# Performance work log

Hardware: AMD Instinct MI355X
Metric: run time of the kernel (lower is better)

The kernel has to match this reference:

```python
import jax, jax.numpy as jnp
import numpy as np

NUM_LAYERS = 6
D = 16           # physical_dim == bond_dim (required for multi-layer consistency)
B, S, FIN = 128, 2048, 128


def setup_inputs() -> dict:
    key = jax.random.key(0)
    k0, k1, k2, k3 = jax.random.split(key, 4)
    return {
        "sequence": jax.random.normal(k0, (B, S, FIN), jnp.float32),
        "W_emb": jax.random.normal(k1, (FIN, D), jnp.float32) * 0.05,
        "b_emb": jnp.zeros((D,), jnp.float32),
        "u": jax.random.normal(k2, (NUM_LAYERS, D, D, D, D), jnp.float32) * 0.1,
        "w": jax.random.normal(k3, (NUM_LAYERS, D, D, D), jnp.float32) * 0.1,
    }


def _ent_entropy(sA, sB):
    # sA: (B, pA, d), sB: (B, pB, d)
    corr = jnp.einsum('bik,bjk->bij', sA, sB)          # (B, pA, pB)
    s = jnp.linalg.svd(corr, compute_uv=False)          # (B, min(pA,pB))
    sn = s / (jnp.sum(s, axis=1, keepdims=True) + 1e-8)
    return -jnp.sum(sn * jnp.log(sn + 1e-8), axis=1)    # (B,)


def _phi_q(sites):
    # sites: (B, n, d), n >= 4 and even
    n = sites.shape[1]
    mid = n // 2
    S_int = _ent_entropy(sites[:, :mid], sites[:, mid:])
    A, Bp = sites[:, :mid], sites[:, mid:]
    S1 = _ent_entropy(A[:, :mid // 2], A[:, mid // 2:])
    S2 = _ent_entropy(Bp[:, :(n - mid) // 2], Bp[:, (n - mid) // 2:])
    return jnp.maximum(S_int - (S1 + S2), 0.0)


def _apply_layer(sites, u_l, w_l):
    # sites: (B, n, d) with n even. Disentangle adjacent pairs, then coarse-grain.
    b, n, d = sites.shape
    s = sites.reshape(b, n // 2, 2, d)
    # disentangler: einsum('ijkl,bi,bj->bkl') batched over pairs p
    comb = jnp.einsum('ijkl,bpi,bpj->bpkl', u_l, s[:, :, 0], s[:, :, 1])
    o1 = comb.mean(axis=3)   # mean over l -> (b, p, k)
    o2 = comb.mean(axis=2)   # mean over k -> (b, p, l)
    # isometry acts on consecutive disentangled pairs (o1_i, o2_i)
    return jnp.einsum('aij,bpi,bpj->bpa', w_l, o1, o2)  # (b, n//2, bond)


def reference(sequence, W_emb, b_emb, u, w):
    emb = sequence @ W_emb + b_emb                       # (B, S, D)
    norm = jnp.linalg.norm(emb, axis=-1, keepdims=True)
    sites = emb / jnp.maximum(norm, 1e-12)               # F.normalize(dim=-1)
    for l in range(NUM_LAYERS):
        sites = _apply_layer(sites, u[l], w[l])
    phi_q = _phi_q(sites)
    return sites, phi_q
```

## Files before the change

### kernel.cpp

```cpp
#include <hip/hip_runtime.h>
#include <hip/hip_bf16.h>
#include <math.h>

#define BATCH 128
#define SEQ   2048
#define FIN   128
#define DD    16
#define NLAYERS 6
#define SST   20
#define SWEEPS 8

#define BUFA_F  (BATCH*SEQ*DD)
#define BUFB_F  (BATCH*(SEQ/2)*DD)
#define COEF_OFF (BUFA_F + BUFB_F)
#define ENT_OFF  (COEF_OFF + NLAYERS*12288)

__global__ __launch_bounds__(256) void k_front(const float* __restrict__ seq,
                                               const float* __restrict__ W,
                                               const float* __restrict__ bias,
                                               const float* __restrict__ u,
                                               const float* __restrict__ w,
                                               float* __restrict__ coef,
                                               float* __restrict__ out) {
    __shared__ float sW[2048];
    __shared__ float sR[64*132];
    int t = threadIdx.x;
    if (blockIdx.x < 6) {
        int l  = blockIdx.x;
        int ij = t;
        const float* ub = u + (size_t)l*65536 + (size_t)ij*256;
        float a1[16], a2[16];
#pragma unroll
        for (int k = 0; k < 16; ++k) { a1[k] = 0.0f; a2[k] = 0.0f; }
#pragma unroll
        for (int k = 0; k < 16; ++k) {
#pragma unroll
            for (int z = 0; z < 16; ++z) {
                float v = ub[k*16 + z];
                a1[k] += v;
                a2[z] += v;
            }
        }
        float* ucb = coef + (size_t)l*12288 + ij*32;
#pragma unroll
        for (int k = 0; k < 16; ++k) {
            ucb[k]      = a1[k]*(1.0f/16.0f);
            ucb[16 + k] = a2[k]*(1.0f/16.0f);
        }
        const float* wb = w + (size_t)l*4096;
        float* wtb = coef + (size_t)l*12288 + 8192 + ij*16;
#pragma unroll
        for (int a = 0; a < 16; ++a) wtb[a] = wb[a*256 + ij];
        return;
    }
    size_t rowbase = (size_t)(blockIdx.x - 6) * 64;
    for (int x = t; x < 2048; x += 256) sW[x] = W[x];
    {
        const float4* seq4 = (const float4*)seq + rowbase*32;
#pragma unroll
        for (int it = 0; it < 8; ++it) {
            int idx = t + it*256;
            int r = idx >> 5, kk = idx & 31;
            *(float4*)&sR[r*132 + kk*4] = seq4[idx];
        }
    }
    int q = t & 3, lr = t >> 2;
    float acc[4];
    {
        float4 bv = *(const float4*)(bias + q*4);
        acc[0] = bv.x; acc[1] = bv.y; acc[2] = bv.z; acc[3] = bv.w;
    }
    __syncthreads();

#pragma unroll 8
    for (int kk = 0; kk < 32; ++kk) {
        float4 rv = *(const float4*)&sR[lr*132 + kk*4];
        float rc[4] = { rv.x, rv.y, rv.z, rv.w };
#pragma unroll
        for (int c = 0; c < 4; ++c) {
            float4 wv = *(const float4*)&sW[(kk*4 + c)*16 + q*4];
            float s = rc[c];
            acc[0] = fmaf(s, wv.x, acc[0]);
            acc[1] = fmaf(s, wv.y, acc[1]);
            acc[2] = fmaf(s, wv.z, acc[2]);
            acc[3] = fmaf(s, wv.w, acc[3]);
        }
    }
    float p = 0.0f;
#pragma unroll
    for (int j = 0; j < 4; ++j) p = fmaf(acc[j], acc[j], p);
    p += __shfl_xor(p, 1);
    p += __shfl_xor(p, 2);
    float inv = 1.0f / fmaxf(sqrtf(p), 1e-12f);
    *(float4*)(out + (rowbase + lr)*16 + q*4) = make_float4(acc[0]*inv, acc[1]*inv,
                                                            acc[2]*inv, acc[3]*inv);
}

__global__ __launch_bounds__(256) void k_layer(const float* __restrict__ in,
                                               float* __restrict__ outp,
                                               const float* __restrict__ coefl) {
    __shared__ float cbuf[8192];
    __shared__ float spl[64*36];
    int t = threadIdx.x;
    int og = t & 7, pg = t >> 3;
    int lane = t & 63, base = lane & ~7;

    const float4* wtf = (const float4*)(coefl + 8192);
    float4 wr0 = wtf[0*256 + t];
    float4 wr1 = wtf[1*256 + t];
    float4 wr2 = wtf[2*256 + t];
    float4 wr3 = wtf[3*256 + t];

    {
        const float4* ucf = (const float4*)coefl;
        float4* c4 = (float4*)cbuf;
#pragma unroll
        for (int it = 0; it < 8; ++it) c4[it*256 + t] = ucf[it*256 + t];
    }
    {
        const float4* ing = (const float4*)in + (size_t)blockIdx.x*512;
        float4 v0 = ing[t];
        float4 v1 = ing[t + 256];
        *(float4*)&spl[(t >> 3)*36 + (t & 7)*4]        = v0;
        *(float4*)&spl[((t >> 3) + 32)*36 + (t & 7)*4] = v1;
    }
    __syncthreads();

    float s1v[2][16];
#pragma unroll
    for (int pp = 0; pp < 2; ++pp) {
        int p = pg + pp*32;
#pragma unroll
        for (int g = 0; g < 4; ++g) {
            float4 v = *(const float4*)&spl[p*36 + 16 + g*4];
            s1v[pp][g*4+0]=v.x; s1v[pp][g*4+1]=v.y; s1v[pp][g*4+2]=v.z; s1v[pp][g*4+3]=v.w;
        }
    }

    float accv[2][4];
    accv[0][0]=0.f; accv[0][1]=0.f; accv[0][2]=0.f; accv[0][3]=0.f;
    accv[1][0]=0.f; accv[1][1]=0.f; accv[1][2]=0.f; accv[1][3]=0.f;

    for (int i = 0; i < 16; ++i) {
        float s0a = spl[pg*36 + i];
        float s0b = spl[(pg + 32)*36 + i];
        const float4* uc = (const float4*)&cbuf[i*512] + og;
#pragma unroll
        for (int j = 0; j < 16; ++j) {
            float4 cv = uc[j*8];
            float pa = s0a * s1v[0][j];
            float pb = s0b * s1v[1][j];
            accv[0][0] = fmaf(pa, cv.x, accv[0][0]);
            accv[0][1] = fmaf(pa, cv.y, accv[0][1]);
            accv[0][2] = fmaf(pa, cv.z, accv[0][2]);
            accv[0][3] = fmaf(pa, cv.w, accv[0][3]);
            accv[1][0] = fmaf(pb, cv.x, accv[1][0]);
            accv[1][1] = fmaf(pb, cv.y, accv[1][1]);
            accv[1][2] = fmaf(pb, cv.z, accv[1][2]);
            accv[1][3] = fmaf(pb, cv.w, accv[1][3]);
        }
    }
    __syncthreads();
    {
        float4* c4 = (float4*)cbuf;
        c4[0*256 + t] = wr0;
        c4[1*256 + t] = wr1;
        c4[2*256 + t] = wr2;
        c4[3*256 + t] = wr3;
    }
    __syncthreads();

    float o2f[2][16];
#pragma unroll
    for (int j = 0; j < 16; ++j) {
        int src = base + 4 + (j >> 2);
        o2f[0][j] = __shfl(accv[0][j & 3], src, 64);
        o2f[1][j] = __shfl(accv[1][j & 3], src, 64);
    }

    float r0a = 0.f, r1a = 0.f, r0b = 0.f, r1b = 0.f;
    for (int grp = 0; grp < 4; ++grp) {
#pragma unroll
        for (int c = 0; c < 4; ++c) {
            float o1a = __shfl(accv[0][c], base + grp, 64);
            float o1b = __shfl(accv[1][c], base + grp, 64);
            const float2* wrow = (const float2*)&cbuf[(grp*4 + c)*256] + og;
#pragma unroll
            for (int j = 0; j < 16; ++j) {
                float2 wv = wrow[j*8];
                float qa = o1a * o2f[0][j];
                float qb = o1b * o2f[1][j];
                r0a = fmaf(qa, wv.x, r0a);
                r1a = fmaf(qa, wv.y, r1a);
                r0b = fmaf(qb, wv.x, r0b);
                r1b = fmaf(qb, wv.y, r1b);
            }
        }
    }

    size_t gp = (size_t)blockIdx.x*64;
    *(float2*)&outp[(gp + pg)*16 + og*2]      = make_float2(r0a, r1a);
    *(float2*)&outp[(gp + pg + 32)*16 + og*2] = make_float2(r0b, r1b);
}

template<int P, bool LAST>
__device__ __forceinline__ void layer_body(float* sL, const float* coef,
                                           float* outp, int npg, int t, int bid) {
    int og = t & 7, pg = t >> 3;
    int lane = t & 63, base = lane & ~7;
    bool act = pg < npg;

    float accv[P][4];
    float s1v[P][16];
#pragma unroll
    for (int pp = 0; pp < P; ++pp) { accv[pp][0]=0.f; accv[pp][1]=0.f; accv[pp][2]=0.f; accv[pp][3]=0.f; }

    if (act) {
#pragma unroll
        for (int pp = 0; pp < P; ++pp) {
            int r = 2*(pg + pp*32) + 1;
#pragma unroll
            for (int g = 0; g < 4; ++g) {
                float4 v = *(const float4*)&sL[r*SST + g*4];
                s1v[pp][g*4+0]=v.x; s1v[pp][g*4+1]=v.y; s1v[pp][g*4+2]=v.z; s1v[pp][g*4+3]=v.w;
            }
        }
        for (int i = 0; i < 16; ++i) {
            float s0[P];
#pragma unroll
            for (int pp = 0; pp < P; ++pp) s0[pp] = sL[(2*(pg + pp*32))*SST + i];
            const float4* uc = (const float4*)&coef[i*512] + og;
#pragma unroll
            for (int j = 0; j < 16; ++j) {
                float4 cv = uc[j*8];
#pragma unroll
                for (int pp = 0; pp < P; ++pp) {
                    float p = s0[pp] * s1v[pp][j];
                    accv[pp][0] = fmaf(p, cv.x, accv[pp][0]);
                    accv[pp][1] = fmaf(p, cv.y, accv[pp][1]);
                    accv[pp][2] = fmaf(p, cv.z, accv[pp][2]);
                    accv[pp][3] = fmaf(p, cv.w, accv[pp][3]);
                }
            }
        }
    }
    __syncthreads();

    if (act) {
        float o2f[P][16];
#pragma unroll
        for (int j = 0; j < 16; ++j) {
            int src = base + 4 + (j >> 2);
#pragma unroll
            for (int pp = 0; pp < P; ++pp)
                o2f[pp][j] = __shfl(accv[pp][j & 3], src, 64);
        }
        float r0[P], r1[P];
#pragma unroll
        for (int pp = 0; pp < P; ++pp) { r0[pp] = 0.f; r1[pp] = 0.f; }
        for (int grp = 0; grp < 4; ++grp) {
#pragma unroll
            for (int c = 0; c < 4; ++c) {
                float o1i[P];
#pragma unroll
                for (int pp = 0; pp < P; ++pp)
                    o1i[pp] = __shfl(accv[pp][c], base + grp, 64);
#pragma unroll
                for (int j = 0; j < 16; ++j) {
                    float2 wv = *(const float2*)&coef[8192 + ((grp*4+c)*16 + j)*16 + og*2];
#pragma unroll
                    for (int pp = 0; pp < P; ++pp) {
                        float q = o1i[pp] * o2f[pp][j];
                        r0[pp] = fmaf(q, wv.x, r0[pp]);
                        r1[pp] = fmaf(q, wv.y, r1[pp]);
                    }
                }
            }
        }
        if (LAST) {
#pragma unroll
            for (int pp = 0; pp < P; ++pp) {
                int p = pg + pp*32;
                *(float2*)&outp[((size_t)bid*32 + p)*16 + og*2] = make_float2(r0[pp], r1[pp]);
            }
        } else {
#pragma unroll
            for (int pp = 0; pp < P; ++pp) {
                int p = pg + pp*32;
                *(float2*)&sL[p*SST + og*2] = make_float2(r0[pp], r1[pp]);
            }
        }
    }
    __syncthreads();
}

__global__ __launch_bounds__(256) void k_tail(const float* __restrict__ in,
                                              const float* __restrict__ coefg,
                                              float* __restrict__ outp) {
    __shared__ float coef[12288];
    __shared__ float sL[256*SST];
    int t = threadIdx.x, bid = blockIdx.x;

    const float4* in4 = (const float4*)in + (size_t)bid*1024;
#pragma unroll
    for (int it = 0; it < 4; ++it) {
        int f = it*256 + t;
        *(float4*)&sL[(f >> 2)*SST + (f & 3)*4] = in4[f];
    }
#pragma unroll 1
    for (int l = 0; l < 3; ++l) {
        const float4* src = (const float4*)(coefg + (size_t)(3 + l)*12288);
        __syncthreads();
        for (int x = t; x < 3072; x += 256) ((float4*)coef)[x] = src[x];
        __syncthreads();
        switch (l) {
            case 0: layer_body<4,false>(sL, coef, outp, 32, t, bid); break;
            case 1: layer_body<2,false>(sL, coef, outp, 32, t, bid); break;
            case 2: layer_body<1,true >(sL, coef, outp, 32, t, bid); break;
        }
    }
}

__device__ __forceinline__ void rot_cs(float al, float be, float ga, float& c, float& s) {
    float ze = (be - al) / (2.0f * ga);
    float tt = copysignf(1.0f, ze) / (fabsf(ze) + sqrtf(1.0f + ze*ze));
    c = 1.0f / sqrtf(1.0f + tt*tt);
    s = c * tt;
}

__global__ __launch_bounds__(64) void k_phi(const float* __restrict__ sites,
                                            float* __restrict__ ent) {
    __shared__ float S[512];
    __shared__ float C[256];
    __shared__ float sv[16];
    int bid = blockIdx.x;
    int role = bid >> 7;
    int b = bid & 127;
    int t = threadIdx.x;
    const float* sp = sites + (size_t)b*512;

    if (role == 0) {
        for (int x = t; x < 512; x += 64) S[x] = sp[x];
        __syncthreads();
        for (int e = t; e < 256; e += 64) {
            int i = e & 15, j = e >> 4;
            float a = 0.0f;
            for (int k = 0; k < 16; ++k) a = fmaf(S[i*16+k], S[(16+j)*16+k], a);
            C[j*16 + i] = a;
        }
        __syncthreads();
        for (int sw = 0; sw < SWEEPS; ++sw) {
            for (int r = 0; r < 15; ++r) {
                int pr = t >> 3, sub = t & 7;
                int p, q;
                if (pr == 0) { p = 15; q = r; }
                else { p = (r + pr) % 15; q = (r + 15 - pr) % 15; }
                float u0 = C[p*16 + 2*sub],   u1v = C[p*16 + 2*sub + 1];
                float v0 = C[q*16 + 2*sub],   v1v = C[q*16 + 2*sub + 1];
                float al = u0*u0 + u1v*u1v;
                float be = v0*v0 + v1v*v1v;
                float ga = u0*v0 + u1v*v1v;
                al += __shfl_xor(al,1); al += __shfl_xor(al,2); al += __shfl_xor(al,4);
                be += __shfl_xor(be,1); be += __shfl_xor(be,2); be += __shfl_xor(be,4);
                ga += __shfl_xor(ga,1); ga += __shfl_xor(ga,2); ga += __shfl_xor(ga,4);
                if (ga != 0.0f) {
                    float c, s; rot_cs(al, be, ga, c, s);
                    C[p*16 + 2*sub]     = fmaf(c, u0, -s*v0);
                    C[p*16 + 2*sub + 1] = fmaf(c, u1v, -s*v1v);
                    C[q*16 + 2*sub]     = fmaf(s, u0,  c*v0);
                    C[q*16 + 2*sub + 1] = fmaf(s, u1v, c*v1v);
                }
                __syncthreads();
            }
        }
        if (t < 16) {
            float s2 = 0.0f;
            for (int rr = 0; rr < 16; ++rr) { float v = C[t*16+rr]; s2 = fmaf(v, v, s2); }
            sv[t] = sqrtf(s2);
        }
        __syncthreads();
        if (t == 0) {
            float sum = 0.0f;
            for (int i2 = 0; i2 < 16; ++i2) sum += sv[i2];
            float den = sum + 1e-8f;
            float e2 = 0.0f;
            for (int i2 = 0; i2 < 16; ++i2) {
                float sn = sv[i2] / den;
                e2 -= sn * logf(sn + 1e-8f);
            }
            ent[b] = e2;
        }
    } else {
        int ro = (role == 1) ? 0 : 256;
        for (int x = t; x < 256; x += 64) S[x] = sp[ro + x];
        __syncthreads();
        if (t < 64) {
            int i = t & 7, j = t >> 3;
            float a = 0.0f;
            for (int k = 0; k < 16; ++k) a = fmaf(S[i*16+k], S[(8+j)*16+k], a);
            C[j*8 + i] = a;
        }
        __syncthreads();
        for (int sw = 0; sw < SWEEPS; ++sw) {
            for (int r = 0; r < 7; ++r) {
                if (t < 32) {
                    int pr = t >> 3, sub = t & 7;
                    int p, q;
                    if (pr == 0) { p = 7; q = r; }
                    else { p = (r + pr) % 7; q = (r + 7 - pr) % 7; }
                    float uu = C[p*8 + sub], vv = C[q*8 + sub];
                    float al = uu*uu, be = vv*vv, ga = uu*vv;
                    al += __shfl_xor(al,1); al += __shfl_xor(al,2); al += __shfl_xor(al,4);
                    be += __shfl_xor(be,1); be += __shfl_xor(be,2); be += __shfl_xor(be,4);
                    ga += __shfl_xor(ga,1); ga += __shfl_xor(ga,2); ga += __shfl_xor(ga,4);
                    if (ga != 0.0f) {
                        float c, s; rot_cs(al, be, ga, c, s);
                        C[p*8 + sub] = fmaf(c, uu, -s*vv);
                        C[q*8 + sub] = fmaf(s, uu,  c*vv);
                    }
                }
                __syncthreads();
            }
        }
        if (t < 8) {
            float s2 = 0.0f;
            for (int rr = 0; rr < 8; ++rr) { float v = C[t*8+rr]; s2 = fmaf(v, v, s2); }
            sv[t] = sqrtf(s2);
        }
        __syncthreads();
        if (t == 0) {
            float sum = 0.0f;
            for (int i2 = 0; i2 < 8; ++i2) sum += sv[i2];
            float den = sum + 1e-8f;
            float e2 = 0.0f;
            for (int i2 = 0; i2 < 8; ++i2) {
                float sn = sv[i2] / den;
                e2 -= sn * logf(sn + 1e-8f);
            }
            ent[role*128 + b] = e2;
        }
    }
}

__global__ __launch_bounds__(128) void k_phi2(const float* __restrict__ ent,
                                              float* __restrict__ phi) {
    int b = threadIdx.x;
    phi[b] = fmaxf(ent[b] - (ent[128 + b] + ent[256 + b]), 0.0f);
}

extern "C" void kernel_launch(void* const* d_in, const int* in_sizes, int n_in,
                              void* d_out, int out_size, void* d_ws, size_t ws_size,
                              hipStream_t stream) {
    const float* seq  = (const float*)d_in[0];
    const float* W    = (const float*)d_in[1];
    const float* bias = (const float*)d_in[2];
    const float* u    = (const float*)d_in[3];
    const float* w    = (const float*)d_in[4];
    float* out = (float*)d_out;
    float* ws  = (float*)d_ws;

    float* bufA  = ws;
    float* bufB  = ws + BUFA_F;
    float* coefw = ws + COEF_OFF;
    float* entb  = ws + ENT_OFF;

    k_front<<<6 + (BATCH*SEQ)/64, 256, 0, stream>>>(seq, W, bias, u, w, coefw, bufA);

    k_layer<<<2048, 256, 0, stream>>>(bufA, bufB, coefw + 0*12288);
    k_layer<<<1024, 256, 0, stream>>>(bufB, bufA, coefw + 1*12288);
    k_layer<<< 512, 256, 0, stream>>>(bufA, bufB, coefw + 2*12288);
    k_tail <<< 128, 256, 0, stream>>>(bufB, coefw, out);

    k_phi <<<3*BATCH, 64, 0, stream>>>(out, entb);
    k_phi2<<<1, 128, 0, stream>>>(entb, out + BATCH*32*DD);
}
```

Baseline: 211.5 us.

## Read sequence rows directly from global memory in embedding kernel, two rows per thread

The embedding front kernel no longer stages 64 input rows in shared memory. Each thread now streams float4s of its rows straight from global memory and computes 4 output columns for two rows, so each block covers 128 rows. The row norm is reduced through a small shared buffer instead of shuffles. This removes the large shared-memory staging and its occupancy cost, but each lane now reads a separate 512-byte row stride, so global loads are poorly coalesced and four waves re-read the same rows.

```diff
diff --git a/kernel.cpp b/kernel.cpp
--- a/kernel.cpp
+++ b/kernel.cpp
@@ -23,7 +23,7 @@
                                                float* __restrict__ coef,
                                                float* __restrict__ out) {
     __shared__ float sW[2048];
-    __shared__ float sR[64*132];
+    __shared__ float psum[128*5 + 4];
     int t = threadIdx.x;
     if (blockIdx.x < 6) {
         int l  = blockIdx.x;
@@ -53,47 +53,52 @@
         for (int a = 0; a < 16; ++a) wtb[a] = wb[a*256 + ij];
         return;
     }
-    size_t rowbase = (size_t)(blockIdx.x - 6) * 64;
-    for (int x = t; x < 2048; x += 256) sW[x] = W[x];
-    {
-        const float4* seq4 = (const float4*)seq + rowbase*32;
-#pragma unroll
-        for (int it = 0; it < 8; ++it) {
-            int idx = t + it*256;
-            int r = idx >> 5, kk = idx & 31;
-            *(float4*)&sR[r*132 + kk*4] = seq4[idx];
-        }
-    }
-    int q = t & 3, lr = t >> 2;
-    float acc[4];
-    {
-        float4 bv = *(const float4*)(bias + q*4);
-        acc[0] = bv.x; acc[1] = bv.y; acc[2] = bv.z; acc[3] = bv.w;
-    }
-    __syncthreads();
-
+    int bid  = blockIdx.x - 6;
+    int lane = t & 63;
+    int q    = t >> 6;
+    for (int x = t; x < 512; x += 256) ((float4*)sW)[x] = ((const float4*)W)[x];
+
+    size_t row0 = (size_t)bid*128 + lane;
+    const float4* rA4 = (const float4*)seq + row0*32;
+    const float4* rB4 = rA4 + 64*32;
+
+    float4 bv = ((const float4*)bias)[q];
+    float a0[4] = { bv.x, bv.y, bv.z, bv.w };
+    float a1[4] = { bv.x, bv.y, bv.z, bv.w };
+    __syncthreads();
+
+    const float4* sW4 = (const float4*)sW;
 #pragma unroll 8
     for (int kk = 0; kk < 32; ++kk) {
-        float4 rv = *(const float4*)&sR[lr*132 + kk*4];
-        float rc[4] = { rv.x, rv.y, rv.z, rv.w };
-#pragma unroll
-        for (int c = 0; c < 4; ++c) {
-            float4 wv = *(const float4*)&sW[(kk*4 + c)*16 + q*4];
-            float s = rc[c];
-            acc[0] = fmaf(s, wv.x, acc[0]);
-            acc[1] = fmaf(s, wv.y, acc[1]);
-            acc[2] = fmaf(s, wv.z, acc[2]);
-            acc[3] = fmaf(s, wv.w, acc[3]);
-        }
-    }
-    float p = 0.0f;
-#pragma unroll
-    for (int j = 0; j < 4; ++j) p = fmaf(acc[j], acc[j], p);
-    p += __shfl_xor(p, 1);
-    p += __shfl_xor(p, 2);
-    float inv = 1.0f / fmaxf(sqrtf(p), 1e-12f);
-    *(float4*)(out + (rowbase + lr)*16 + q*4) = make_float4(acc[0]*inv, acc[1]*inv,
-                                                            acc[2]*inv, acc[3]*inv);
+        float4 rA = rA4[kk];
+        float4 rB = rB4[kk];
+        float4 w0 = sW4[(kk*4 + 0)*4 + q];
+        float4 w1 = sW4[(kk*4 + 1)*4 + q];
+        float4 w2 = sW4[(kk*4 + 2)*4 + q];
+        float4 w3 = sW4[(kk*4 + 3)*4 + q];
+        a0[0]=fmaf(rA.x,w0.x,a0[0]); a0[1]=fmaf(rA.x,w0.y,a0[1]); a0[2]=fmaf(rA.x,w0.z,a0[2]); a0[3]=fmaf(rA.x,w0.w,a0[3]);
+        a0[0]=fmaf(rA.y,w1.x,a0[0]); a0[1]=fmaf(rA.y,w1.y,a0[1]); a0[2]=fmaf(rA.y,w1.z,a0[2]); a0[3]=fmaf(rA.y,w1.w,a0[3]);
+        a0[0]=fmaf(rA.z,w2.x,a0[0]); a0[1]=fmaf(rA.z,w2.y,a0[1]); a0[2]=fmaf(rA.z,w2.z,a0[2]); a0[3]=fmaf(rA.z,w2.w,a0[3]);
+        a0[0]=fmaf(rA.w,w3.x,a0[0]); a0[1]=fmaf(rA.w,w3.y,a0[1]); a0[2]=fmaf(rA.w,w3.z,a0[2]); a0[3]=fmaf(rA.w,w3.w,a0[3]);
+        a1[0]=fmaf(rB.x,w0.x,a1[0]); a1[1]=fmaf(rB.x,w0.y,a1[1]); a1[2]=fmaf(rB.x,w0.z,a1[2]); a1[3]=fmaf(rB.x,w0.w,a1[3]);
+        a1[0]=fmaf(rB.y,w1.x,a1[0]); a1[1]=fmaf(rB.y,w1.y,a1[1]); a1[2]=fmaf(rB.y,w1.z,a1[2]); a1[3]=fmaf(rB.y,w1.w,a1[3]);
+        a1[0]=fmaf(rB.z,w2.x,a1[0]); a1[1]=fmaf(rB.z,w2.y,a1[1]); a1[2]=fmaf(rB.z,w2.z,a1[2]); a1[3]=fmaf(rB.z,w2.w,a1[3]);
+        a1[0]=fmaf(rB.w,w3.x,a1[0]); a1[1]=fmaf(rB.w,w3.y,a1[1]); a1[2]=fmaf(rB.w,w3.z,a1[2]); a1[3]=fmaf(rB.w,w3.w,a1[3]);
+    }
+    {
+        float p0 = 0.f, p1 = 0.f;
+#pragma unroll
+        for (int j = 0; j < 4; ++j) { p0 = fmaf(a0[j], a0[j], p0); p1 = fmaf(a1[j], a1[j], p1); }
+        psum[lane*5 + q]      = p0;
+        psum[(lane+64)*5 + q] = p1;
+    }
+    __syncthreads();
+    float s0 = ((psum[lane*5+0] + psum[lane*5+1]) + psum[lane*5+2]) + psum[lane*5+3];
+    float s1 = ((psum[(lane+64)*5+0] + psum[(lane+64)*5+1]) + psum[(lane+64)*5+2]) + psum[(lane+64)*5+3];
+    float inv0 = 1.0f / fmaxf(sqrtf(s0), 1e-12f);
+    float inv1 = 1.0f / fmaxf(sqrtf(s1), 1e-12f);
+    *(float4*)(out + row0*16 + q*4)      = make_float4(a0[0]*inv0, a0[1]*inv0, a0[2]*inv0, a0[3]*inv0);
+    *(float4*)(out + (row0+64)*16 + q*4) = make_float4(a1[0]*inv1, a1[1]*inv1, a1[2]*inv1, a1[3]*inv1);
 }
 
 __global__ __launch_bounds__(256) void k_layer(const float* __restrict__ in,
@@ -464,7 +469,7 @@
     float* coefw = ws + COEF_OFF;
     float* entb  = ws + ENT_OFF;
 
-    k_front<<<6 + (BATCH*SEQ)/64, 256, 0, stream>>>(seq, W, bias, u, w, coefw, bufA);
+    k_front<<<6 + (BATCH*SEQ)/128, 256, 0, stream>>>(seq, W, bias, u, w, coefw, bufA);
 
     k_layer<<<2048, 256, 0, stream>>>(bufA, bufB, coefw + 0*12288);
     k_layer<<<1024, 256, 0, stream>>>(bufB, bufA, coefw + 1*12288);
```

After: 244.0 us. 1.15x slower.

## Restructure embedding kernel into two half-tile passes and widen layer blocks to 512 threads

Applied to the files above, without the earlier changes.

The embedding front kernel now stages 32 rows at a time through a half-size shared buffer over two passes. Each row is computed by 8 threads producing 2 outputs each instead of 4 threads producing 4, which cuts LDS use and per-thread registers to allow more resident blocks. The layer kernel moves to 512-thread blocks covering 128 pairs, so the shared coefficient table is loaded into LDS once per twice as many pairs. The cost is extra barriers in the front kernel and fewer, larger layer blocks that may lower occupancy.

```diff
diff --git a/kernel.cpp b/kernel.cpp
--- a/kernel.cpp
+++ b/kernel.cpp
@@ -23,7 +23,7 @@
                                                float* __restrict__ coef,
                                                float* __restrict__ out) {
     __shared__ float sW[2048];
-    __shared__ float sR[64*132];
+    __shared__ float sR[32*132];
     int t = threadIdx.x;
     if (blockIdx.x < 6) {
         int l  = blockIdx.x;
@@ -54,82 +54,81 @@
         return;
     }
     size_t rowbase = (size_t)(blockIdx.x - 6) * 64;
-    for (int x = t; x < 2048; x += 256) sW[x] = W[x];
     {
-        const float4* seq4 = (const float4*)seq + rowbase*32;
-#pragma unroll
-        for (int it = 0; it < 8; ++it) {
-            int idx = t + it*256;
-            int r = idx >> 5, kk = idx & 31;
-            *(float4*)&sR[r*132 + kk*4] = seq4[idx];
-        }
-    }
-    int q = t & 3, lr = t >> 2;
-    float acc[4];
-    {
-        float4 bv = *(const float4*)(bias + q*4);
-        acc[0] = bv.x; acc[1] = bv.y; acc[2] = bv.z; acc[3] = bv.w;
-    }
-    __syncthreads();
-
+        const float4* W4 = (const float4*)W;
+        float4* s4 = (float4*)sW;
+        s4[t]       = W4[t];
+        s4[t + 256] = W4[t + 256];
+    }
+    int og = t & 7, r = t >> 3;
+    float2 bv = *(const float2*)(bias + 2*og);
+    const float4* sR4 = (const float4*)sR;
+
+#pragma unroll 1
+    for (int ps = 0; ps < 2; ++ps) {
+        {
+            const float4* seq4 = (const float4*)seq + (rowbase + ps*32)*32;
+#pragma unroll
+            for (int it = 0; it < 4; ++it) {
+                int idx = it*256 + t;
+                *(float4*)&sR[(idx >> 5)*132 + (idx & 31)*4] = seq4[idx];
+            }
+        }
+        __syncthreads();
+        float acc0 = bv.x, acc1 = bv.y;
 #pragma unroll 8
-    for (int kk = 0; kk < 32; ++kk) {
-        float4 rv = *(const float4*)&sR[lr*132 + kk*4];
-        float rc[4] = { rv.x, rv.y, rv.z, rv.w };
-#pragma unroll
-        for (int c = 0; c < 4; ++c) {
-            float4 wv = *(const float4*)&sW[(kk*4 + c)*16 + q*4];
-            float s = rc[c];
-            acc[0] = fmaf(s, wv.x, acc[0]);
-            acc[1] = fmaf(s, wv.y, acc[1]);
-            acc[2] = fmaf(s, wv.z, acc[2]);
-            acc[3] = fmaf(s, wv.w, acc[3]);
-        }
-    }
-    float p = 0.0f;
-#pragma unroll
-    for (int j = 0; j < 4; ++j) p = fmaf(acc[j], acc[j], p);
-    p += __shfl_xor(p, 1);
-    p += __shfl_xor(p, 2);
-    float inv = 1.0f / fmaxf(sqrtf(p), 1e-12f);
-    *(float4*)(out + (rowbase + lr)*16 + q*4) = make_float4(acc[0]*inv, acc[1]*inv,
-                                                            acc[2]*inv, acc[3]*inv);
-}
-
-__global__ __launch_bounds__(256) void k_layer(const float* __restrict__ in,
+        for (int kk = 0; kk < 32; ++kk) {
+            float4 rv = sR4[r*33 + kk];
+            float rc[4] = { rv.x, rv.y, rv.z, rv.w };
+#pragma unroll
+            for (int c = 0; c < 4; ++c) {
+                float2 wv = *(const float2*)&sW[(kk*4 + c)*16 + 2*og];
+                acc0 = fmaf(rc[c], wv.x, acc0);
+                acc1 = fmaf(rc[c], wv.y, acc1);
+            }
+        }
+        float p = fmaf(acc0, acc0, acc1*acc1);
+        p += __shfl_xor(p, 1);
+        p += __shfl_xor(p, 2);
+        p += __shfl_xor(p, 4);
+        float inv = 1.0f / fmaxf(sqrtf(p), 1e-12f);
+        *(float2*)(out + (rowbase + ps*32 + r)*16 + 2*og) = make_float2(acc0*inv, acc1*inv);
+        __syncthreads();
+    }
+}
+
+__global__ __launch_bounds__(512) void k_layer(const float* __restrict__ in,
                                                float* __restrict__ outp,
                                                const float* __restrict__ coefl) {
     __shared__ float cbuf[8192];
-    __shared__ float spl[64*36];
+    __shared__ float spl[128*36];
     int t = threadIdx.x;
     int og = t & 7, pg = t >> 3;
     int lane = t & 63, base = lane & ~7;
 
     const float4* wtf = (const float4*)(coefl + 8192);
-    float4 wr0 = wtf[0*256 + t];
-    float4 wr1 = wtf[1*256 + t];
-    float4 wr2 = wtf[2*256 + t];
-    float4 wr3 = wtf[3*256 + t];
+    float4 wr0 = wtf[t];
+    float4 wr1 = wtf[t + 512];
 
     {
         const float4* ucf = (const float4*)coefl;
         float4* c4 = (float4*)cbuf;
 #pragma unroll
-        for (int it = 0; it < 8; ++it) c4[it*256 + t] = ucf[it*256 + t];
+        for (int it = 0; it < 4; ++it) c4[it*512 + t] = ucf[it*512 + t];
     }
     {
-        const float4* ing = (const float4*)in + (size_t)blockIdx.x*512;
+        const float4* ing = (const float4*)in + (size_t)blockIdx.x*1024;
         float4 v0 = ing[t];
-        float4 v1 = ing[t + 256];
-        *(float4*)&spl[(t >> 3)*36 + (t & 7)*4]        = v0;
-        *(float4*)&spl[((t >> 3) + 32)*36 + (t & 7)*4] = v1;
+        float4 v1 = ing[t + 512];
+        *(float4*)&spl[(t >> 3)*36 + (t & 7)*4]         = v0;
+        *(float4*)&spl[((t >> 3) + 64)*36 + (t & 7)*4]  = v1;
     }
     __syncthreads();
 
     float s1v[2][16];
 #pragma unroll
     for (int pp = 0; pp < 2; ++pp) {
-        int p = pg + pp*32;
+        int p = pg + pp*64;
 #pragma unroll
         for (int g = 0; g < 4; ++g) {
             float4 v = *(const float4*)&spl[p*36 + 16 + g*4];
@@ -143,7 +142,7 @@
 
     for (int i = 0; i < 16; ++i) {
         float s0a = spl[pg*36 + i];
-        float s0b = spl[(pg + 32)*36 + i];
+        float s0b = spl[(pg + 64)*36 + i];
         const float4* uc = (const float4*)&cbuf[i*512] + og;
 #pragma unroll
         for (int j = 0; j < 16; ++j) {
@@ -163,10 +162,8 @@
     __syncthreads();
     {
         float4* c4 = (float4*)cbuf;
-        c4[0*256 + t] = wr0;
-        c4[1*256 + t] = wr1;
-        c4[2*256 + t] = wr2;
-        c4[3*256 + t] = wr3;
+        c4[t]       = wr0;
+        c4[t + 512] = wr1;
     }
     __syncthreads();
 
@@ -198,9 +195,9 @@
         }
     }
 
-    size_t gp = (size_t)blockIdx.x*64;
+    size_t gp = (size_t)blockIdx.x*128;
     *(float2*)&outp[(gp + pg)*16 + og*2]      = make_float2(r0a, r1a);
-    *(float2*)&outp[(gp + pg + 32)*16 + og*2] = make_float2(r0b, r1b);
+    *(float2*)&outp[(gp + pg + 64)*16 + og*2] = make_float2(r0b, r1b);
 }
 
 template<int P, bool LAST>
@@ -466,9 +463,9 @@
 
     k_front<<<6 + (BATCH*SEQ)/64, 256, 0, stream>>>(seq, W, bias, u, w, coefw, bufA);
 
-    k_layer<<<2048, 256, 0, stream>>>(bufA, bufB, coefw + 0*12288);
-    k_layer<<<1024, 256, 0, stream>>>(bufB, bufA, coefw + 1*12288);
-    k_layer<<< 512, 256, 0, stream>>>(bufA, bufB, coefw + 2*12288);
+    k_layer<<<1024, 512, 0, stream>>>(bufA, bufB, coefw + 0*12288);
+    k_layer<<< 512, 512, 0, stream>>>(bufB, bufA, coefw + 1*12288);
+    k_layer<<< 256, 512, 0, stream>>>(bufA, bufB, coefw + 2*12288);
     k_tail <<< 128, 256, 0, stream>>>(bufB, coefw, out);
 
     k_phi <<<3*BATCH, 64, 0, stream>>>(out, entb);
```

Measured after the change: 219.5 us. 1.04x slower.

## Restructure embedding kernel: 128-thread blocks, two row passes, two rows per thread

Applied to the files above, without the earlier changes.

The embedding/normalize kernel now uses 128-thread blocks that each handle 128 rows in two 64-row passes. Each thread computes two rows, so every shared-memory W load is reused across both rows, and W is staged only once per 128 rows. This halves the block count and the W staging work. In exchange, each block serializes two load-then-compute phases with barriers, which may reduce latency hiding on this memory-bound stream of sequence data.

```diff
diff --git a/kernel.cpp b/kernel.cpp
--- a/kernel.cpp
+++ b/kernel.cpp
@@ -15,7 +15,7 @@
 #define COEF_OFF (BUFA_F + BUFB_F)
 #define ENT_OFF  (COEF_OFF + NLAYERS*12288)
 
-__global__ __launch_bounds__(256) void k_front(const float* __restrict__ seq,
+__global__ __launch_bounds__(128) void k_front(const float* __restrict__ seq,
                                                const float* __restrict__ W,
                                                const float* __restrict__ bias,
                                                const float* __restrict__ u,
@@ -26,74 +26,90 @@
     __shared__ float sR[64*132];
     int t = threadIdx.x;
     if (blockIdx.x < 6) {
-        int l  = blockIdx.x;
-        int ij = t;
-        const float* ub = u + (size_t)l*65536 + (size_t)ij*256;
-        float a1[16], a2[16];
-#pragma unroll
-        for (int k = 0; k < 16; ++k) { a1[k] = 0.0f; a2[k] = 0.0f; }
-#pragma unroll
-        for (int k = 0; k < 16; ++k) {
-#pragma unroll
-            for (int z = 0; z < 16; ++z) {
-                float v = ub[k*16 + z];
-                a1[k] += v;
-                a2[z] += v;
-            }
-        }
-        float* ucb = coef + (size_t)l*12288 + ij*32;
-#pragma unroll
-        for (int k = 0; k < 16; ++k) {
-            ucb[k]      = a1[k]*(1.0f/16.0f);
-            ucb[16 + k] = a2[k]*(1.0f/16.0f);
-        }
-        const float* wb = w + (size_t)l*4096;
-        float* wtb = coef + (size_t)l*12288 + 8192 + ij*16;
-#pragma unroll
-        for (int a = 0; a < 16; ++a) wtb[a] = wb[a*256 + ij];
+        int l = blockIdx.x;
+        for (int ij = t; ij < 256; ij += 128) {
+            const float* ub = u + (size_t)l*65536 + (size_t)ij*256;
+            float a1[16], a2[16];
+#pragma unroll
+            for (int k = 0; k < 16; ++k) { a1[k] = 0.0f; a2[k] = 0.0f; }
+#pragma unroll
+            for (int k = 0; k < 16; ++k) {
+#pragma unroll
+                for (int z = 0; z < 16; ++z) {
+                    float v = ub[k*16 + z];
+                    a1[k] += v;
+                    a2[z] += v;
+                }
+            }
+            float* ucb = coef + (size_t)l*12288 + ij*32;
+#pragma unroll
+            for (int k = 0; k < 16; ++k) {
+                ucb[k]      = a1[k]*(1.0f/16.0f);
+                ucb[16 + k] = a2[k]*(1.0f/16.0f);
+            }
+            const float* wb = w + (size_t)l*4096;
+            float* wtb = coef + (size_t)l*12288 + 8192 + ij*16;
+#pragma unroll
+            for (int a = 0; a < 16; ++a) wtb[a] = wb[a*256 + ij];
+        }
         return;
     }
-    size_t rowbase = (size_t)(blockIdx.x - 6) * 64;
-    for (int x = t; x < 2048; x += 256) sW[x] = W[x];
+    size_t rowbase = (size_t)(blockIdx.x - 6) * 128;
     {
-        const float4* seq4 = (const float4*)seq + rowbase*32;
-#pragma unroll
-        for (int it = 0; it < 8; ++it) {
-            int idx = t + it*256;
-            int r = idx >> 5, kk = idx & 31;
-            *(float4*)&sR[r*132 + kk*4] = seq4[idx];
-        }
-    }
-    int q = t & 3, lr = t >> 2;
-    float acc[4];
-    {
-        float4 bv = *(const float4*)(bias + q*4);
-        acc[0] = bv.x; acc[1] = bv.y; acc[2] = bv.z; acc[3] = bv.w;
-    }
-    __syncthreads();
-
-#pragma unroll 8
-    for (int kk = 0; kk < 32; ++kk) {
-        float4 rv = *(const float4*)&sR[lr*132 + kk*4];
-        float rc[4] = { rv.x, rv.y, rv.z, rv.w };
-#pragma unroll
-        for (int c = 0; c < 4; ++c) {
-            float4 wv = *(const float4*)&sW[(kk*4 + c)*16 + q*4];
-            float s = rc[c];
-            acc[0] = fmaf(s, wv.x, acc[0]);
-            acc[1] = fmaf(s, wv.y, acc[1]);
-            acc[2] = fmaf(s, wv.z, acc[2]);
-            acc[3] = fmaf(s, wv.w, acc[3]);
-        }
-    }
-    float p = 0.0f;
-#pragma unroll
-    for (int j = 0; j < 4; ++j) p = fmaf(acc[j], acc[j], p);
-    p += __shfl_xor(p, 1);
-    p += __shfl_xor(p, 2);
-    float inv = 1.0f / fmaxf(sqrtf(p), 1e-12f);
-    *(float4*)(out + (rowbase + lr)*16 + q*4) = make_float4(acc[0]*inv, acc[1]*inv,
-                                                            acc[2]*inv, acc[3]*inv);
+        const float4* W4 = (const float4*)W;
+        float4* s4 = (float4*)sW;
+#pragma unroll
+        for (int it = 0; it < 4; ++it) s4[it*128 + t] = W4[it*128 + t];
+    }
+    int q = t & 3, g = t >> 2;
+    float4 bv = *(const float4*)(bias + q*4);
+    const float4* sR4 = (const float4*)sR;
+    const float4* sW4 = (const float4*)sW;
+
+#pragma unroll 1
+    for (int ps = 0; ps < 2; ++ps) {
+        {
+            const float4* seq4 = (const float4*)seq + (rowbase + ps*64)*32;
+#pragma unroll
+            for (int it = 0; it < 16; ++it) {
+                int idx = it*128 + t;
+                *(float4*)&sR[(idx >> 5)*132 + (idx & 31)*4] = seq4[idx];
+            }
+        }
+        __syncthreads();
+        float a0[4] = { bv.x, bv.y, bv.z, bv.w };
+        float a1[4] = { bv.x, bv.y, bv.z, bv.w };
+#pragma unroll 4
+        for (int kk = 0; kk < 32; ++kk) {
+            float4 r0 = sR4[g*33 + kk];
+            float4 r1 = sR4[(g + 32)*33 + kk];
+            float rc0[4] = { r0.x, r0.y, r0.z, r0.w };
+            float rc1[4] = { r1.x, r1.y, r1.z, r1.w };
+#pragma unroll
+            for (int c = 0; c < 4; ++c) {
+                float4 wv = sW4[(kk*4 + c)*4 + q];
+                a0[0] = fmaf(rc0[c], wv.x, a0[0]);
+                a0[1] = fmaf(rc0[c], wv.y, a0[1]);
+                a0[2] = fmaf(rc0[c], wv.z, a0[2]);
+                a0[3] = fmaf(rc0[c], wv.w, a0[3]);
+                a1[0] = fmaf(rc1[c], wv.x, a1[0]);
+                a1[1] = fmaf(rc1[c], wv.y, a1[1]);
+                a1[2] = fmaf(rc1[c], wv.z, a1[2]);
+                a1[3] = fmaf(rc1[c], wv.w, a1[3]);
+            }
+        }
+        float p0 = 0.0f, p1 = 0.0f;
+#pragma unroll
+        for (int j = 0; j < 4; ++j) { p0 = fmaf(a0[j], a0[j], p0); p1 = fmaf(a1[j], a1[j], p1); }
+        p0 += __shfl_xor(p0, 1); p0 += __shfl_xor(p0, 2);
+        p1 += __shfl_xor(p1, 1); p1 += __shfl_xor(p1, 2);
+        float inv0 = 1.0f / fmaxf(sqrtf(p0), 1e-12f);
+        float inv1 = 1.0f / fmaxf(sqrtf(p1), 1e-12f);
+        size_t r0w = rowbase + ps*64 + g;
+        *(float4*)(out + r0w*16 + q*4)        = make_float4(a0[0]*inv0, a0[1]*inv0, a0[2]*inv0, a0[3]*inv0);
+        *(float4*)(out + (r0w + 32)*16 + q*4) = make_float4(a1[0]*inv1, a1[1]*inv1, a1[2]*inv1, a1[3]*inv1);
+        __syncthreads();
+    }
 }
 
 __global__ __launch_bounds__(256) void k_layer(const float* __restrict__ in,
@@ -464,7 +480,7 @@
     float* coefw = ws + COEF_OFF;
     float* entb  = ws + ENT_OFF;
 
-    k_front<<<6 + (BATCH*SEQ)/64, 256, 0, stream>>>(seq, W, bias, u, w, coefw, bufA);
+    k_front<<<6 + (BATCH*SEQ)/128, 128, 0, stream>>>(seq, W, bias, u, w, coefw, bufA);
 
     k_layer<<<2048, 256, 0, stream>>>(bufA, bufB, coefw + 0*12288);
     k_layer<<<1024, 256, 0, stream>>>(bufB, bufA, coefw + 1*12288);
```

After: 206.7 us. -2.2%, faster.
